# Kernel optimization log

Hardware: AMD Instinct MI355X
Metric: run time of the kernel (lower is better)

The kernel has to match this reference:

```python
import jax, jax.numpy as jnp
import numpy as np

RRF_K = 60.0
NUM_DOCS = 1_000_000


def setup_inputs() -> dict:
    key = jax.random.key(0)
    k1, k2, k3 = jax.random.split(key, 3)
    B, T, K = 60, 4, 100
    return {
        "index_tensor": jax.random.randint(k1, (B, T, K), 0, NUM_DOCS, dtype=jnp.int64 if jax.config.jax_enable_x64 else jnp.int32).astype(jnp.int32),
        "ranking_tensor": jax.random.uniform(k2, (B, T, K), dtype=jnp.float32),
        "weight": jnp.ones((T,), dtype=jnp.float32),
        "pos_positions": jax.random.randint(k3, (B,), 0, 5, dtype=jnp.int32),
        "num_docs": NUM_DOCS,
    }


def reference(index_tensor, ranking_tensor, weight, pos_positions, num_docs):
    # index_tensor: [B, T, K] doc ids; ranking_tensor: [B, T, K] teacher scores/ranks
    B = index_tensor.shape[0]
    # weighted reciprocal-rank-fusion score per retrieved doc: w_t / (RRF_K + rank)
    rrf = weight[None, :, None] / (RRF_K + ranking_tensor)  # [B, T, K]
    flat_idx = index_tensor.reshape(B, -1)                  # [B, T*K]
    flat_s = rrf.reshape(B, -1)                             # [B, T*K]
    # batched scatter-add into the per-query fused score vector [B, num_docs]
    fused = jnp.zeros((B, num_docs), dtype=ranking_tensor.dtype)
    fused = fused.at[jnp.arange(B)[:, None], flat_idx].add(flat_s)
    # full descending argsort per query (torch.argsort(..., descending=True))
    order = jnp.argsort(-fused, axis=1)                     # [B, num_docs]
    positive_idx = order[jnp.arange(B), pos_positions]      # [B]
    return order, positive_idx
```

## Files before the change

kernel.cpp:

```cpp
#include <hip/hip_runtime.h>
#include <hip/hip_bf16.h>

#define T_DIM 4
#define K_DIM 100
#define NPER 400
#define NDOCS 1000000
#define FILL_BLOCK 256
#define FILL_PER_THREAD 16
#define FILL_CHUNK (FILL_BLOCK * FILL_PER_THREAD)
#define BLOCKS_PER_ROW ((NDOCS + FILL_CHUNK - 1) / FILL_CHUNK)

__global__ __launch_bounds__(512) void rrf_prep_kernel(
    const int* __restrict__ idx, const float* __restrict__ rnk,
    const float* __restrict__ weight, const int* __restrict__ pos,
    int* __restrict__ wsA, int* __restrict__ wsHead, int* __restrict__ wsNnz,
    int* __restrict__ out_pos)
{
  const int b = blockIdx.x;
  const int tid = threadIdx.x;
  const int lane = tid & 63, wave = tid >> 6;

  __shared__ int   ids[NPER];
  __shared__ float sc[NPER];
  __shared__ int   sid[NPER];
  __shared__ float ssc[NPER];
  __shared__ int   uid[NPER];
  __shared__ float usc[NPER];
  __shared__ int   head[NPER];
  __shared__ int   wsum[8];

  if (tid < NPER) {
    ids[tid] = idx[b * NPER + tid];
    sc[tid]  = weight[tid / K_DIM] / (60.0f + rnk[b * NPER + tid]);
  }
  __syncthreads();

  if (tid < NPER) {
    const int myid = ids[tid];
    int r = 0;
    for (int j = 0; j < NPER; ++j) {
      const int oj = ids[j];
      r += (oj < myid) || (oj == myid && j < tid);
    }
    sid[r] = myid;
    ssc[r] = sc[tid];
  }
  __syncthreads();

  int isLeader = 0;
  float mysum = 0.0f;
  if (tid < NPER) {
    isLeader = (tid == 0) || (sid[tid] != sid[tid - 1]);
    if (isLeader) {
      mysum = ssc[tid];
      for (int k = tid + 1; k < NPER && sid[k] == sid[tid]; ++k) mysum += ssc[k];
    }
  }

  int val = isLeader;
#pragma unroll
  for (int off = 1; off < 64; off <<= 1) {
    int n = __shfl_up(val, off, 64);
    if (lane >= off) val += n;
  }
  if (lane == 63) wsum[wave] = val;
  __syncthreads();
  if (wave == 0 && lane < 8) {
    int wv = wsum[lane];
#pragma unroll
    for (int off = 1; off < 8; off <<= 1) {
      int n = __shfl_up(wv, off, 8);
      if ((lane & 7) >= off) wv += n;
    }
    wsum[lane] = wv;
  }
  __syncthreads();
  const int incl = val + (wave > 0 ? wsum[wave - 1] : 0);
  const int nnz  = wsum[7];

  if (isLeader) {
    const int u = incl - 1;
    uid[u] = sid[tid];
    usc[u] = mysum;
  }
  __syncthreads();

  if (tid < nnz) {
    const float si = usc[tid];
    const int   ii = uid[tid];
    int r2 = 0;
    for (int j = 0; j < nnz; ++j) {
      const float sj = usc[j];
      r2 += (sj > si) || (sj == si && uid[j] < ii);
    }
    head[r2] = ii;
  }
  __syncthreads();

  if (tid < nnz) {
    wsA[b * NPER + tid]    = uid[tid] - tid;
    wsHead[b * NPER + tid] = head[tid];
  }
  if (tid == 0) {
    wsNnz[b]   = nnz;
    out_pos[b] = head[pos[b]];
  }
}

__global__ __launch_bounds__(FILL_BLOCK) void rrf_fill_kernel(
    const int* __restrict__ wsA, const int* __restrict__ wsHead,
    const int* __restrict__ wsNnz, int* __restrict__ out)
{
  const int row   = blockIdx.x / BLOCKS_PER_ROW;
  const int chunk = blockIdx.x % BLOCKS_PER_ROW;
  const int tid   = threadIdx.x;

  __shared__ int A[NPER];
  __shared__ int H[NPER];
  __shared__ int s_nnz;

  for (int i = tid; i < NPER; i += FILL_BLOCK)
    A[i] = wsA[row * NPER + i];
  if (chunk == 0)
    for (int i = tid; i < NPER; i += FILL_BLOCK)
      H[i] = wsHead[row * NPER + i];
  if (tid == 0) s_nnz = wsNnz[row];
  __syncthreads();
  const int nnz = s_nnz;

  const int chunkbase = chunk * FILL_CHUNK;
  int* outrow = out + (long long)row * NDOCS;

  if (chunkbase >= nnz && chunk + 1 < BLOCKS_PER_ROW) {
#pragma unroll
    for (int q = 0; q < 4; ++q) {
      const int p0 = chunkbase + q * 1024 + tid * 4;
      int z = p0 - nnz;
      int lo = 0, hi = nnz;
      while (lo < hi) { const int mid = (lo + hi) >> 1; if (A[mid] <= z) lo = mid + 1; else hi = mid; }
      int j = lo;
      int4 pk;
      pk.x = z + j;
      ++z; while (j < nnz && A[j] <= z) ++j; pk.y = z + j;
      ++z; while (j < nnz && A[j] <= z) ++j; pk.z = z + j;
      ++z; while (j < nnz && A[j] <= z) ++j; pk.w = z + j;
      *reinterpret_cast<int4*>(outrow + p0) = pk;
    }
  } else {
#pragma unroll
    for (int q = 0; q < 4; ++q) {
      const int p0 = chunkbase + q * 1024 + tid * 4;
      if (p0 >= NDOCS) continue;
      int vv[4];
#pragma unroll
      for (int k = 0; k < 4; ++k) {
        const int p = p0 + k;
        if (p < nnz) vv[k] = H[p];
        else {
          const int z = p - nnz;
          int lo = 0, hi = nnz;
          while (lo < hi) { const int mid = (lo + hi) >> 1; if (A[mid] <= z) lo = mid + 1; else hi = mid; }
          vv[k] = z + lo;
        }
      }
      *reinterpret_cast<int4*>(outrow + p0) = make_int4(vv[0], vv[1], vv[2], vv[3]);
    }
  }
}

extern "C" void kernel_launch(void* const* d_in, const int* in_sizes, int n_in,
                              void* d_out, int out_size, void* d_ws, size_t ws_size,
                              hipStream_t stream) {
  const int*   idx    = (const int*)d_in[0];
  const float* rnk    = (const float*)d_in[1];
  const float* weight = (const float*)d_in[2];
  const int*   pos    = (const int*)d_in[3];
  const int B = in_sizes[3];

  int* out = (int*)d_out;
  int* ws  = (int*)d_ws;
  int* wsA    = ws;
  int* wsHead = ws + (size_t)B * NPER;
  int* wsNnz  = ws + (size_t)2 * B * NPER;

  rrf_prep_kernel<<<B, 512, 0, stream>>>(idx, rnk, weight, pos,
                                         wsA, wsHead, wsNnz,
                                         out + (size_t)B * NDOCS);
  rrf_fill_kernel<<<B * BLOCKS_PER_ROW, FILL_BLOCK, 0, stream>>>(wsA, wsHead, wsNnz, out);
}
```

Measured before the change: 288.3 us.

## Replace per-thread binary search with block-wide range count in fill kernel

Doubles the elements each fill thread writes and, for chunks past the head region, finds once per block the range of excluded-doc offsets that fall in the chunk. Each thread then computes its outputs by counting over that small range with branch-free comparisons instead of running a binary search per four-element group. This is meant to cut divergent shared-memory search loops and halve the block count, in exchange for fewer blocks in flight and more registers per thread.

```diff
diff --git a/kernel.cpp b/kernel.cpp
--- a/kernel.cpp
+++ b/kernel.cpp
@@ -6,9 +6,10 @@
 #define NPER 400
 #define NDOCS 1000000
 #define FILL_BLOCK 256
-#define FILL_PER_THREAD 16
+#define FILL_PER_THREAD 32
 #define FILL_CHUNK (FILL_BLOCK * FILL_PER_THREAD)
 #define BLOCKS_PER_ROW ((NDOCS + FILL_CHUNK - 1) / FILL_CHUNK)
+#define QN (FILL_PER_THREAD / 4)
 
 __global__ __launch_bounds__(512) void rrf_prep_kernel(
     const int* __restrict__ idx, const float* __restrict__ rnk,
@@ -132,23 +133,41 @@
   int* outrow = out + (long long)row * NDOCS;
 
   if (chunkbase >= nnz && chunk + 1 < BLOCKS_PER_ROW) {
-#pragma unroll
-    for (int q = 0; q < 4; ++q) {
-      const int p0 = chunkbase + q * 1024 + tid * 4;
-      int z = p0 - nnz;
-      int lo = 0, hi = nnz;
-      while (lo < hi) { const int mid = (lo + hi) >> 1; if (A[mid] <= z) lo = mid + 1; else hi = mid; }
-      int j = lo;
-      int4 pk;
-      pk.x = z + j;
-      ++z; while (j < nnz && A[j] <= z) ++j; pk.y = z + j;
-      ++z; while (j < nnz && A[j] <= z) ++j; pk.z = z + j;
-      ++z; while (j < nnz && A[j] <= z) ++j; pk.w = z + j;
-      *reinterpret_cast<int4*>(outrow + p0) = pk;
-    }
+    const int z0   = chunkbase - nnz;
+    const int zend = z0 + FILL_CHUNK - 1;
+
+    int lo = 0, hi = nnz;
+    while (lo < hi) { const int mid = (lo + hi) >> 1; if (A[mid] < z0) lo = mid + 1; else hi = mid; }
+    const int j0 = lo;
+    hi = nnz;
+    while (lo < hi) { const int mid = (lo + hi) >> 1; if (A[mid] <= zend) lo = mid + 1; else hi = mid; }
+    const int j1 = lo;
+
+    const int za = z0 + tid * 4;
+    int v[QN][4];
+#pragma unroll
+    for (int q = 0; q < QN; ++q) {
+      const int b = za + q * 1024 + j0;
+      v[q][0] = b; v[q][1] = b + 1; v[q][2] = b + 2; v[q][3] = b + 3;
+    }
+    for (int k = j0; k < j1; ++k) {
+      const int a = A[k];
+#pragma unroll
+      for (int q = 0; q < QN; ++q) {
+        const int z = za + q * 1024;
+        v[q][0] += (a <= z);
+        v[q][1] += (a <= z + 1);
+        v[q][2] += (a <= z + 2);
+        v[q][3] += (a <= z + 3);
+      }
+    }
+#pragma unroll
+    for (int q = 0; q < QN; ++q)
+      *reinterpret_cast<int4*>(outrow + chunkbase + q * 1024 + tid * 4) =
+          make_int4(v[q][0], v[q][1], v[q][2], v[q][3]);
   } else {
 #pragma unroll
-    for (int q = 0; q < 4; ++q) {
+    for (int q = 0; q < QN; ++q) {
       const int p0 = chunkbase + q * 1024 + tid * 4;
       if (p0 >= NDOCS) continue;
       int vv[4];
```

Result: slower. 297.9 us (+3.3%).
